# Kernel optimization log

Hardware: AMD Instinct MI355X
Metric: run time of the kernel (lower is better)

The kernel has to match this reference:

```python
import jax, jax.numpy as jnp
import numpy as np

EPS = 1e-8  # torch CosineSimilarity default eps


def setup_inputs() -> dict:
    key = jax.random.key(0)
    k_emb, k_ei, k_w1, k_w2, k_b1, k_b2 = jax.random.split(key, 6)
    N, H, E = 50000, 256, 300000
    emb = jax.random.normal(k_emb, (N, H), dtype=jnp.float32)
    edge_index = jax.random.randint(k_ei, (2, E), 0, N, dtype=jnp.int64)
    # Xavier-uniform init for the two Linear layers (fan_in = fan_out = H)
    limit = float(np.sqrt(6.0 / (H + H)))
    W1 = jax.random.uniform(k_w1, (H, H), minval=-limit, maxval=limit, dtype=jnp.float32)
    W2 = jax.random.uniform(k_w2, (H, H), minval=-limit, maxval=limit, dtype=jnp.float32)
    b1 = jnp.zeros((H,), dtype=jnp.float32)
    b2 = jnp.zeros((H,), dtype=jnp.float32)
    return {"emb": emb, "edge_index": edge_index, "W1": W1, "b1": b1, "W2": W2, "b2": b2}


def _mlp(x, W1, b1, W2, b2):
    # Linear -> Dropout(eval: identity) -> ReLU -> Linear
    h = jax.nn.relu(x @ W1.T + b1)
    return h @ W2.T + b2


def _cosine(a, b):
    # torch.nn.CosineSimilarity(dim=1): dot / (max(||a||, eps) * max(||b||, eps))
    dot = jnp.sum(a * b, axis=1)
    na = jnp.maximum(jnp.linalg.norm(a, axis=1), EPS)
    nb = jnp.maximum(jnp.linalg.norm(b, axis=1), EPS)
    return dot / (na * nb)


def reference(emb, edge_index, W1, b1, W2, b2):
    col, row = edge_index[0], edge_index[1]
    f1 = emb[col]  # [E, H]
    f2 = emb[row]  # [E, H]
    g1 = _mlp(f1, W1, b1, W2, b2)
    g2 = _mlp(f2, W1, b1, W2, b2)
    return _cosine(g1, g2)  # [E] per-edge attention logits
```

## Files before the change

### kernel.cpp

```cpp
#include <hip/hip_runtime.h>
#include <stdint.h>

#define H 256
#define EPS 1e-8f

typedef __bf16 bf16x8 __attribute__((ext_vector_type(8)));
typedef float  f32x4  __attribute__((ext_vector_type(4)));

__device__ __forceinline__ unsigned short f2bf(float f) {
  unsigned u = __builtin_bit_cast(unsigned, f);
  u += 0x7FFFu + ((u >> 16) & 1u);
  return (unsigned short)(u >> 16);
}
__device__ __forceinline__ float bflo(unsigned u){ return __builtin_bit_cast(float, u << 16); }
__device__ __forceinline__ float bfhi(unsigned u){ return __builtin_bit_cast(float, u & 0xFFFF0000u); }

__global__ __launch_bounds__(256) void conv_w_kernel(
    const float* __restrict__ W1, const float* __restrict__ W2,
    unsigned short* __restrict__ w1B, unsigned short* __restrict__ w2B) {
  int i = (blockIdx.x * 256 + threadIdx.x) * 4;
  const int HH = H * H;
  if (i >= 2 * HH) return;
  const float* s = (i < HH) ? W1 : W2;
  unsigned short* d = (i < HH) ? w1B : w2B;
  int j = (i < HH) ? i : i - HH;
  float4 v = *(const float4*)(s + j);
  ushort4 o;
  o.x = f2bf(v.x); o.y = f2bf(v.y); o.z = f2bf(v.z); o.w = f2bf(v.w);
  *(ushort4*)(d + j) = o;
}

__global__ __launch_bounds__(256) void fused_mlp_kernel(
    const float* __restrict__ Af,
    const unsigned short* __restrict__ W1,
    const unsigned short* __restrict__ W2,
    const float* __restrict__ b1, const float* __restrict__ b2,
    unsigned short* __restrict__ G,
    float* __restrict__ rn, int N) {
  __shared__ unsigned short sA[2][64 * 32];
  __shared__ unsigned short sW[2][256 * 32];
  __shared__ unsigned short sH[64 * 256];
  __shared__ float ssb[64][2];

  const int tid  = threadIdx.x;
  const int wave = tid >> 6, lane = tid & 63;
  const int quad = lane >> 4, l16 = lane & 15;
  const int wr = wave >> 1, wn = wave & 1;
  const size_t bm = blockIdx.x;

  const int arow = tid >> 2, kch = (tid & 3) * 8;
  const int grow = (int)bm * 64 + arow;
  const bool avalid = grow < N;
  const int crow = avalid ? grow : (N - 1);
  const float* gAf = Af + (size_t)crow * H + kch;
  const unsigned short* gW1 = W1 + (size_t)arow * H + kch;
  const unsigned short* gW2 = W2 + (size_t)arow * H + kch;

  const float4 z4 = make_float4(0.f, 0.f, 0.f, 0.f);
  float4 rf[3][2];
  uint4  rw[2][4];

#define LOADA(kt, s)                                                            \
  do {                                                                          \
    rf[s][0] = *(const float4*)(gAf + (kt) * 32);                               \
    rf[s][1] = *(const float4*)(gAf + (kt) * 32 + 4);                           \
  } while (0)
#define WRITEA(s, buf)                                                          \
  do {                                                                          \
    float4 t0 = avalid ? rf[s][0] : z4;                                         \
    float4 t1 = avalid ? rf[s][1] : z4;                                         \
    uint4 p;                                                                    \
    p.x = (unsigned)f2bf(t0.x) | ((unsigned)f2bf(t0.y) << 16);                  \
    p.y = (unsigned)f2bf(t0.z) | ((unsigned)f2bf(t0.w) << 16);                  \
    p.z = (unsigned)f2bf(t1.x) | ((unsigned)f2bf(t1.y) << 16);                  \
    p.w = (unsigned)f2bf(t1.z) | ((unsigned)f2bf(t1.w) << 16);                  \
    *(uint4*)(&sA[buf][tid * 8]) = p;                                           \
  } while (0)
#define LOADW(gW, kt, s)                                                        \
  do {                                                                          \
    _Pragma("unroll")                                                           \
    for (int c = 0; c < 4; c++)                                                 \
      rw[s][c] = *(const uint4*)((gW) + (size_t)(c * 64) * H + (kt) * 32);      \
  } while (0)
#define WRITEW(s, buf)                                                          \
  do {                                                                          \
    _Pragma("unroll")                                                           \
    for (int c = 0; c < 4; c++)                                                 \
      *(uint4*)(&sW[buf][c * 2048 + tid * 8]) = rw[s][c];                       \
  } while (0)
#define LGKM_BAR()                                                              \
  do {                                                                          \
    asm volatile("s_waitcnt lgkmcnt(0)" ::: "memory");                          \
    __builtin_amdgcn_s_barrier();                                               \
  } while (0)

  f32x4 acc[8][2];
#pragma unroll
  for (int i = 0; i < 8; i++)
#pragma unroll
    for (int j = 0; j < 2; j++) acc[i][j] = (f32x4){0.f, 0.f, 0.f, 0.f};

  LOADW(gW1, 0, 0);
  LOADW(gW1, 1, 1);
  LOADA(0, 0); LOADA(1, 1); LOADA(2, 2);
  WRITEW(0, 0);
  WRITEA(0, 0);
  LGKM_BAR();

#pragma unroll
  for (int kt = 0; kt < 8; ++kt) {
    if (kt) LGKM_BAR();
    if (kt < 6) LOADW(gW1, kt + 2, kt & 1);
    if (kt == 6) LOADW(gW2, 0, 0);
    if (kt == 7) LOADW(gW2, 1, 1);
    if (kt < 5) LOADA(kt + 3, kt % 3);

    bf16x8 wf[8], af0, af1;
#pragma unroll
    for (int i = 0; i < 8; i++)
      wf[i] = *(const bf16x8*)(&sW[kt & 1][(wn * 128 + i * 16 + l16) * 32 + quad * 8]);
    af0 = *(const bf16x8*)(&sA[kt & 1][(wr * 32 + 0 * 16 + l16) * 32 + quad * 8]);
    af1 = *(const bf16x8*)(&sA[kt & 1][(wr * 32 + 1 * 16 + l16) * 32 + quad * 8]);

    if (kt < 7) {
      WRITEW((kt + 1) & 1, (kt + 1) & 1);
      WRITEA((kt + 1) % 3, (kt + 1) & 1);
    } else {
      WRITEW(0, 0);
    }

#pragma unroll
    for (int i = 0; i < 8; i++) {
      acc[i][0] = __builtin_amdgcn_mfma_f32_16x16x32_bf16(wf[i], af0, acc[i][0], 0, 0, 0);
      acc[i][1] = __builtin_amdgcn_mfma_f32_16x16x32_bf16(wf[i], af1, acc[i][1], 0, 0, 0);
    }
  }

#pragma unroll
  for (int i = 0; i < 8; i++) {
    const int hcol = wn * 128 + i * 16 + quad * 4;
    const float4 bv = *(const float4*)(b1 + hcol);
#pragma unroll
    for (int j = 0; j < 2; j++) {
      const int row = wr * 32 + j * 16 + l16;
      f32x4 v = acc[i][j];
      unsigned short h0 = f2bf(fmaxf(v[0] + bv.x, 0.f));
      unsigned short h1 = f2bf(fmaxf(v[1] + bv.y, 0.f));
      unsigned short h2 = f2bf(fmaxf(v[2] + bv.z, 0.f));
      unsigned short h3 = f2bf(fmaxf(v[3] + bv.w, 0.f));
      uint2 p;
      p.x = (unsigned)h0 | ((unsigned)h1 << 16);
      p.y = (unsigned)h2 | ((unsigned)h3 << 16);
      unsigned off = (unsigned)(row * 512 + hcol * 2) ^ ((unsigned)(row & 7) << 4);
      *(uint2*)((char*)sH + off) = p;
    }
  }

  LGKM_BAR();

  f32x4 acc2[2][8];
#pragma unroll
  for (int i = 0; i < 2; i++)
#pragma unroll
    for (int j = 0; j < 8; j++) acc2[i][j] = (f32x4){0.f, 0.f, 0.f, 0.f};

#pragma unroll
  for (int kt = 0; kt < 8; ++kt) {
    if (kt) LGKM_BAR();
    if (kt < 6) LOADW(gW2, kt + 2, kt & 1);

    bf16x8 wf2[8], hf[2];
#pragma unroll
    for (int j = 0; j < 8; j++)
      wf2[j] = *(const bf16x8*)(&sW[kt & 1][(wn * 128 + j * 16 + l16) * 32 + quad * 8]);
#pragma unroll
    for (int i = 0; i < 2; i++) {
      const int hrow = wr * 32 + i * 16 + l16;
      unsigned off = (unsigned)(hrow * 512 + kt * 64 + quad * 16) ^ ((unsigned)(hrow & 7) << 4);
      hf[i] = *(const bf16x8*)((const char*)sH + off);
    }

    if (kt < 7) WRITEW((kt + 1) & 1, (kt + 1) & 1);

#pragma unroll
    for (int i = 0; i < 2; i++)
#pragma unroll
      for (int j = 0; j < 8; j++)
        acc2[i][j] = __builtin_amdgcn_mfma_f32_16x16x32_bf16(hf[i], wf2[j], acc2[i][j], 0, 0, 0);
  }

  float b2v[8];
#pragma unroll
  for (int j = 0; j < 8; j++) b2v[j] = b2[wn * 128 + j * 16 + l16];
#pragma unroll
  for (int i = 0; i < 2; i++)
#pragma unroll
    for (int j = 0; j < 8; j++)
#pragma unroll
      for (int r = 0; r < 4; r++) acc2[i][j][r] += b2v[j];

  float ss[2][4];
#pragma unroll
  for (int i = 0; i < 2; i++)
#pragma unroll
    for (int r = 0; r < 4; r++) {
      float s = 0.f;
#pragma unroll
      for (int j = 0; j < 8; j++) s += acc2[i][j][r] * acc2[i][j][r];
      ss[i][r] = s;
    }
#pragma unroll
  for (int m = 1; m < 16; m <<= 1)
#pragma unroll
    for (int i = 0; i < 2; i++)
#pragma unroll
      for (int r = 0; r < 4; r++) ss[i][r] += __shfl_xor(ss[i][r], m, 64);
  if (l16 == 0) {
#pragma unroll
    for (int i = 0; i < 2; i++)
#pragma unroll
      for (int r = 0; r < 4; r++) ssb[wr * 32 + i * 16 + quad * 4 + r][wn] = ss[i][r];
  }
  __syncthreads();
  if (tid < 64) {
    float s2 = ssb[tid][0] + ssb[tid][1];
    rn[bm * 64 + tid] = 1.f / fmaxf(sqrtf(s2), EPS);
  }

#pragma unroll
  for (int i = 0; i < 2; i++)
#pragma unroll
    for (int j = 0; j < 8; j++) {
      const int gcol = wn * 128 + j * 16 + l16;
#pragma unroll
      for (int r = 0; r < 4; r++) {
        const size_t grow2 = bm * 64 + wr * 32 + i * 16 + quad * 4 + r;
        G[grow2 * H + gcol] = f2bf(acc2[i][j][r]);
      }
    }
#undef LOADA
#undef WRITEA
#undef LOADW
#undef WRITEW
#undef LGKM_BAR
}

__device__ __forceinline__ float dot_u4(uint4 a, uint4 b) {
  float s;
  s  = bflo(a.x) * bflo(b.x) + bfhi(a.x) * bfhi(b.x);
  s += bflo(a.y) * bflo(b.y) + bfhi(a.y) * bfhi(b.y);
  s += bflo(a.z) * bflo(b.z) + bfhi(a.z) * bfhi(b.z);
  s += bflo(a.w) * bflo(b.w) + bfhi(a.w) * bfhi(b.w);
  return s;
}

__global__ __launch_bounds__(256) void edge_cos_kernel(
    const int* __restrict__ ei, const unsigned short* __restrict__ g,
    const float* __restrict__ rn, float* __restrict__ out, int E) {
  const int lane = threadIdx.x & 63;
  const int wid  = threadIdx.x >> 6;
  const int l8   = lane & 7;
  const int sub  = lane >> 3;
  const int e    = blockIdx.x * 32 + wid * 8 + sub;
  if (e >= E) return;
  const int c = ei[e], r = ei[E + e];
  const uint4* gc = (const uint4*)(g + (size_t)c * H);
  const uint4* gr = (const uint4*)(g + (size_t)r * H);
  uint4 a0 = gc[l8], a1 = gc[l8 + 8], a2 = gc[l8 + 16], a3 = gc[l8 + 24];
  uint4 b0 = gr[l8], b1 = gr[l8 + 8], b2 = gr[l8 + 16], b3 = gr[l8 + 24];
  float d = dot_u4(a0, b0) + dot_u4(a1, b1) + dot_u4(a2, b2) + dot_u4(a3, b3);
  d += __shfl_xor(d, 4, 8);
  d += __shfl_xor(d, 2, 8);
  d += __shfl_xor(d, 1, 8);
  if (l8 == 0) out[e] = d * rn[c] * rn[r];
}

extern "C" void kernel_launch(void* const* d_in, const int* in_sizes, int n_in,
                              void* d_out, int out_size, void* d_ws, size_t ws_size,
                              hipStream_t stream) {
  const float* emb = (const float*)d_in[0];
  const int*   ei  = (const int*)d_in[1];
  const float* W1  = (const float*)d_in[2];
  const float* b1  = (const float*)d_in[3];
  const float* W2  = (const float*)d_in[4];
  const float* b2  = (const float*)d_in[5];
  float* out = (float*)d_out;

  const int NH = in_sizes[0];
  const int N  = NH / H;
  const int E  = in_sizes[1] / 2;
  const int Mp = ((N + 63) / 64) * 64;

  char* ws = (char*)d_ws;
  unsigned short* gB   = (unsigned short*)ws; ws += (size_t)Mp * H * 2;
  unsigned short* w1B  = (unsigned short*)ws; ws += (size_t)H * H * 2;
  unsigned short* w2B  = (unsigned short*)ws; ws += (size_t)H * H * 2;
  float* rn            = (float*)ws;

  conv_w_kernel<<<(2 * H * H / 4 + 255) / 256, 256, 0, stream>>>(W1, W2, w1B, w2B);

  fused_mlp_kernel<<<Mp / 64, 256, 0, stream>>>(emb, w1B, w2B, b1, b2, gB, rn, N);

  edge_cos_kernel<<<(E + 31) / 32, 256, 0, stream>>>(ei, gB, rn, out, E);
}
```

Before: 170.1 us.

## Pre-swizzle weights into MFMA fragment order and load directly to registers

The weight conversion kernel now writes W1/W2 in bf16 in the exact per-lane MFMA fragment order, so the MLP kernel loads weight fragments straight from global/L2 into registers with double buffering instead of staging them through shared memory. This removes the weight LDS buffer, its writes and reads, and frees LDS (ssb now aliases sA, with an added barrier), which may raise occupancy. In exchange every block re-reads weights from cache with 16-byte per-lane loads, and the register footprint grows with two sets of eight bf16x8 fragments.

```diff
diff --git a/kernel.cpp b/kernel.cpp
--- a/kernel.cpp
+++ b/kernel.cpp
@@ -15,32 +15,42 @@
 __device__ __forceinline__ float bflo(unsigned u){ return __builtin_bit_cast(float, u << 16); }
 __device__ __forceinline__ float bfhi(unsigned u){ return __builtin_bit_cast(float, u & 0xFFFF0000u); }
 
+__device__ __forceinline__ uint4 pack8(float4 a, float4 b) {
+  uint4 p;
+  p.x = (unsigned)f2bf(a.x) | ((unsigned)f2bf(a.y) << 16);
+  p.y = (unsigned)f2bf(a.z) | ((unsigned)f2bf(a.w) << 16);
+  p.z = (unsigned)f2bf(b.x) | ((unsigned)f2bf(b.y) << 16);
+  p.w = (unsigned)f2bf(b.z) | ((unsigned)f2bf(b.w) << 16);
+  return p;
+}
+
 __global__ __launch_bounds__(256) void conv_w_kernel(
     const float* __restrict__ W1, const float* __restrict__ W2,
-    unsigned short* __restrict__ w1B, unsigned short* __restrict__ w2B) {
-  int i = (blockIdx.x * 256 + threadIdx.x) * 4;
-  const int HH = H * H;
-  if (i >= 2 * HH) return;
-  const float* s = (i < HH) ? W1 : W2;
-  unsigned short* d = (i < HH) ? w1B : w2B;
-  int j = (i < HH) ? i : i - HH;
-  float4 v = *(const float4*)(s + j);
-  ushort4 o;
-  o.x = f2bf(v.x); o.y = f2bf(v.y); o.z = f2bf(v.z); o.w = f2bf(v.w);
-  *(ushort4*)(d + j) = o;
+    unsigned short* __restrict__ w1S, unsigned short* __restrict__ w2S) {
+  int t = blockIdx.x * 256 + threadIdx.x;
+  if (t >= 2 * 8192) return;
+  const float* src = (t < 8192) ? W1 : W2;
+  unsigned short* dst = (t < 8192) ? w1S : w2S;
+  int g = t & 8191;
+  int wn = g >> 12, rem = g & 4095, f = rem >> 6, lane = rem & 63;
+  int kt = f >> 3, i = f & 7, l16 = lane & 15, quad = lane >> 4;
+  int row = wn * 128 + i * 16 + l16;
+  int k0  = kt * 32 + quad * 8;
+  float4 a = *(const float4*)(src + (size_t)row * H + k0);
+  float4 b = *(const float4*)(src + (size_t)row * H + k0 + 4);
+  *(uint4*)(dst + (size_t)g * 8) = pack8(a, b);
 }
 
 __global__ __launch_bounds__(256) void fused_mlp_kernel(
     const float* __restrict__ Af,
-    const unsigned short* __restrict__ W1,
-    const unsigned short* __restrict__ W2,
+    const unsigned short* __restrict__ W1S,
+    const unsigned short* __restrict__ W2S,
     const float* __restrict__ b1, const float* __restrict__ b2,
     unsigned short* __restrict__ G,
     float* __restrict__ rn, int N) {
   __shared__ unsigned short sA[2][64 * 32];
-  __shared__ unsigned short sW[2][256 * 32];
   __shared__ unsigned short sH[64 * 256];
-  __shared__ float ssb[64][2];
+  float (*ssb)[2] = (float(*)[2])sA;
 
   const int tid  = threadIdx.x;
   const int wave = tid >> 6, lane = tid & 63;
@@ -53,40 +63,29 @@
   const bool avalid = grow < N;
   const int crow = avalid ? grow : (N - 1);
   const float* gAf = Af + (size_t)crow * H + kch;
-  const unsigned short* gW1 = W1 + (size_t)arow * H + kch;
-  const unsigned short* gW2 = W2 + (size_t)arow * H + kch;
+  const unsigned short* w1p = W1S + ((size_t)wn * 4096 + lane) * 8;
+  const unsigned short* w2p = W2S + ((size_t)wn * 4096 + lane) * 8;
 
   const float4 z4 = make_float4(0.f, 0.f, 0.f, 0.f);
-  float4 rf[3][2];
-  uint4  rw[2][4];
+  float4 rf[2][2];
+  bf16x8 wreg[2][8];
 
 #define LOADA(kt, s)                                                            \
   do {                                                                          \
     rf[s][0] = *(const float4*)(gAf + (kt) * 32);                               \
     rf[s][1] = *(const float4*)(gAf + (kt) * 32 + 4);                           \
   } while (0)
-#define WRITEA(s, buf)                                                          \
+#define WRITEA(s)                                                               \
   do {                                                                          \
     float4 t0 = avalid ? rf[s][0] : z4;                                         \
     float4 t1 = avalid ? rf[s][1] : z4;                                         \
-    uint4 p;                                                                    \
-    p.x = (unsigned)f2bf(t0.x) | ((unsigned)f2bf(t0.y) << 16);                  \
-    p.y = (unsigned)f2bf(t0.z) | ((unsigned)f2bf(t0.w) << 16);                  \
-    p.z = (unsigned)f2bf(t1.x) | ((unsigned)f2bf(t1.y) << 16);                  \
-    p.w = (unsigned)f2bf(t1.z) | ((unsigned)f2bf(t1.w) << 16);                  \
-    *(uint4*)(&sA[buf][tid * 8]) = p;                                           \
-  } while (0)
-#define LOADW(gW, kt, s)                                                        \
+    *(uint4*)(&sA[s][tid * 8]) = pack8(t0, t1);                                 \
+  } while (0)
+#define LOADWF(buf, wp, kt)                                                     \
   do {                                                                          \
     _Pragma("unroll")                                                           \
-    for (int c = 0; c < 4; c++)                                                 \
-      rw[s][c] = *(const uint4*)((gW) + (size_t)(c * 64) * H + (kt) * 32);      \
-  } while (0)
-#define WRITEW(s, buf)                                                          \
-  do {                                                                          \
-    _Pragma("unroll")                                                           \
-    for (int c = 0; c < 4; c++)                                                 \
-      *(uint4*)(&sW[buf][c * 2048 + tid * 8]) = rw[s][c];                       \
+    for (int i_ = 0; i_ < 8; i_++)                                              \
+      wreg[buf][i_] = *(const bf16x8*)((wp) + ((kt) * 8 + i_) * 512);           \
   } while (0)
 #define LGKM_BAR()                                                              \
   do {                                                                          \
@@ -100,40 +99,33 @@
 #pragma unroll
     for (int j = 0; j < 2; j++) acc[i][j] = (f32x4){0.f, 0.f, 0.f, 0.f};
 
-  LOADW(gW1, 0, 0);
-  LOADW(gW1, 1, 1);
-  LOADA(0, 0); LOADA(1, 1); LOADA(2, 2);
-  WRITEW(0, 0);
-  WRITEA(0, 0);
+  LOADWF(0, w1p, 0);
+  LOADWF(1, w1p, 1);
+  LOADA(0, 0);
+  LOADA(1, 1);
+  WRITEA(0);
   LGKM_BAR();
 
 #pragma unroll
   for (int kt = 0; kt < 8; ++kt) {
-    if (kt) LGKM_BAR();
-    if (kt < 6) LOADW(gW1, kt + 2, kt & 1);
-    if (kt == 6) LOADW(gW2, 0, 0);
-    if (kt == 7) LOADW(gW2, 1, 1);
-    if (kt < 5) LOADA(kt + 3, kt % 3);
-
-    bf16x8 wf[8], af0, af1;
-#pragma unroll
-    for (int i = 0; i < 8; i++)
-      wf[i] = *(const bf16x8*)(&sW[kt & 1][(wn * 128 + i * 16 + l16) * 32 + quad * 8]);
+    if (kt < 6) LOADA(kt + 2, kt & 1);
+    if (kt < 7) WRITEA((kt + 1) & 1);
+
+    bf16x8 af0, af1;
     af0 = *(const bf16x8*)(&sA[kt & 1][(wr * 32 + 0 * 16 + l16) * 32 + quad * 8]);
     af1 = *(const bf16x8*)(&sA[kt & 1][(wr * 32 + 1 * 16 + l16) * 32 + quad * 8]);
 
-    if (kt < 7) {
-      WRITEW((kt + 1) & 1, (kt + 1) & 1);
-      WRITEA((kt + 1) % 3, (kt + 1) & 1);
-    } else {
-      WRITEW(0, 0);
-    }
-
 #pragma unroll
     for (int i = 0; i < 8; i++) {
-      acc[i][0] = __builtin_amdgcn_mfma_f32_16x16x32_bf16(wf[i], af0, acc[i][0], 0, 0, 0);
-      acc[i][1] = __builtin_amdgcn_mfma_f32_16x16x32_bf16(wf[i], af1, acc[i][1], 0, 0, 0);
-    }
+      acc[i][0] = __builtin_amdgcn_mfma_f32_16x16x32_bf16(wreg[kt & 1][i], af0, acc[i][0], 0, 0, 0);
+      acc[i][1] = __builtin_amdgcn_mfma_f32_16x16x32_bf16(wreg[kt & 1][i], af1, acc[i][1], 0, 0, 0);
+    }
+
+    if (kt < 6)       LOADWF(kt & 1, w1p, kt + 2);
+    else if (kt == 6) LOADWF(0, w2p, 0);
+    else              LOADWF(1, w2p, 1);
+
+    if (kt < 7) LGKM_BAR();
   }
 
 #pragma unroll
@@ -166,27 +158,19 @@
 
 #pragma unroll
   for (int kt = 0; kt < 8; ++kt) {
-    if (kt) LGKM_BAR();
-    if (kt < 6) LOADW(gW2, kt + 2, kt & 1);
-
-    bf16x8 wf2[8], hf[2];
-#pragma unroll
-    for (int j = 0; j < 8; j++)
-      wf2[j] = *(const bf16x8*)(&sW[kt & 1][(wn * 128 + j * 16 + l16) * 32 + quad * 8]);
+    bf16x8 hf[2];
 #pragma unroll
     for (int i = 0; i < 2; i++) {
       const int hrow = wr * 32 + i * 16 + l16;
       unsigned off = (unsigned)(hrow * 512 + kt * 64 + quad * 16) ^ ((unsigned)(hrow & 7) << 4);
       hf[i] = *(const bf16x8*)((const char*)sH + off);
     }
-
-    if (kt < 7) WRITEW((kt + 1) & 1, (kt + 1) & 1);
-
 #pragma unroll
     for (int i = 0; i < 2; i++)
 #pragma unroll
       for (int j = 0; j < 8; j++)
-        acc2[i][j] = __builtin_amdgcn_mfma_f32_16x16x32_bf16(hf[i], wf2[j], acc2[i][j], 0, 0, 0);
+        acc2[i][j] = __builtin_amdgcn_mfma_f32_16x16x32_bf16(hf[i], wreg[kt & 1][j], acc2[i][j], 0, 0, 0);
+    if (kt < 6) LOADWF(kt & 1, w2p, kt + 2);
   }
 
   float b2v[8];
@@ -215,6 +199,7 @@
     for (int i = 0; i < 2; i++)
 #pragma unroll
       for (int r = 0; r < 4; r++) ss[i][r] += __shfl_xor(ss[i][r], m, 64);
+  __syncthreads();
   if (l16 == 0) {
 #pragma unroll
     for (int i = 0; i < 2; i++)
@@ -240,8 +225,7 @@
     }
 #undef LOADA
 #undef WRITEA
-#undef LOADW
-#undef WRITEW
+#undef LOADWF
 #undef LGKM_BAR
 }
 
@@ -293,13 +277,13 @@
 
   char* ws = (char*)d_ws;
   unsigned short* gB   = (unsigned short*)ws; ws += (size_t)Mp * H * 2;
-  unsigned short* w1B  = (unsigned short*)ws; ws += (size_t)H * H * 2;
-  unsigned short* w2B  = (unsigned short*)ws; ws += (size_t)H * H * 2;
+  unsigned short* w1S  = (unsigned short*)ws; ws += (size_t)H * H * 2;
+  unsigned short* w2S  = (unsigned short*)ws; ws += (size_t)H * H * 2;
   float* rn            = (float*)ws;
 
-  conv_w_kernel<<<(2 * H * H / 4 + 255) / 256, 256, 0, stream>>>(W1, W2, w1B, w2B);
-
-  fused_mlp_kernel<<<Mp / 64, 256, 0, stream>>>(emb, w1B, w2B, b1, b2, gB, rn, N);
+  conv_w_kernel<<<64, 256, 0, stream>>>(W1, W2, w1S, w2S);
+
+  fused_mlp_kernel<<<Mp / 64, 256, 0, stream>>>(emb, w1S, w2S, b1, b2, gB, rn, N);
 
   edge_cos_kernel<<<(E + 31) / 32, 256, 0, stream>>>(ei, gB, rn, out, E);
 }
```

After: 156.5 us. 8.0% less time.
